# Kernel tuning notes

Measured on AMD Instinct MI355X. Metric: run time of the kernel, lower is better.

The kernel has to match this reference:

```python
import jax, jax.numpy as jnp
import numpy as np

EMBED_DIM = 768
NUM_HEADS = 12
HEAD_DIM = EMBED_DIM // NUM_HEADS
MAX_WAVELENGTH = 10000.0
ROPE_PERCENT = 0.5


def p_rope(x, positions):
    """Partial RoPE (Gemma-style half-split layout) on x: [BH, S, D]."""
    rope_angles = int(ROPE_PERCENT * HEAD_DIM) // 2
    nope_angles = HEAD_DIM // 2 - rope_angles
    fraction = 2.0 * jnp.arange(rope_angles, dtype=x.dtype) / HEAD_DIM
    timescale = MAX_WAVELENGTH ** fraction
    # infinite timescale => angle 0 => identity rotation for the non-roped dims
    timescale = jnp.concatenate([timescale, jnp.full((nope_angles,), jnp.inf, dtype=x.dtype)])
    sinusoid = positions[:, None] / timescale[None, :]  # [S, D/2]
    sin, cos = jnp.sin(sinusoid), jnp.cos(sinusoid)
    x1, x2 = jnp.split(x, 2, axis=-1)  # each [BH, S, D/2]
    return jnp.concatenate([x1 * cos - x2 * sin, x2 * cos + x1 * sin], axis=-1)


def setup_inputs() -> dict:
    key = jax.random.key(0)
    ks = jax.random.split(key, 9)
    B, T, E = 16, 1024, EMBED_DIM
    s = 0.02
    return {
        "hidden_states": jax.random.normal(ks[0], (B, T, E), jnp.float32),
        "wq": jax.random.normal(ks[1], (E, E), jnp.float32) * s,
        "bq": jax.random.normal(ks[2], (E,), jnp.float32) * s,
        "wk": jax.random.normal(ks[3], (E, E), jnp.float32) * s,
        "bk": jax.random.normal(ks[4], (E,), jnp.float32) * s,
        "wv": jax.random.normal(ks[5], (E, E), jnp.float32) * s,
        "bv": jax.random.normal(ks[6], (E,), jnp.float32) * s,
        "wo": jax.random.normal(ks[7], (E, E), jnp.float32) * s,
        "bo": jax.random.normal(ks[8], (E,), jnp.float32) * s,
    }


def _shape(x, B, S):
    # [B, S, E] -> [B*H, S, head_dim]
    return x.reshape(B, S, NUM_HEADS, HEAD_DIM).transpose(0, 2, 1, 3).reshape(B * NUM_HEADS, S, HEAD_DIM)


def reference(hidden_states, wq, bq, wk, bk, wv, bv, wo, bo):
    B, T, E = hidden_states.shape
    scaling = HEAD_DIM ** -0.5
    # torch nn.Linear: y = x @ W.T + b
    q = (hidden_states @ wq.T + bq) * scaling
    k = hidden_states @ wk.T + bk
    v = hidden_states @ wv.T + bv
    q = _shape(q, B, T)  # [BH, T, D]
    k = _shape(k, B, T)
    v = _shape(v, B, T)
    positions = jnp.arange(T, dtype=hidden_states.dtype)
    k = p_rope(k, positions)
    q = p_rope(q, positions)
    attn = jnp.einsum('bqd,bkd->bqk', q, k)  # [BH, T, T]
    attn = jax.nn.softmax(attn, axis=-1)
    out = jnp.einsum('bqk,bkd->bqd', attn, v)  # [BH, T, D]
    out = out.reshape(B, NUM_HEADS, T, HEAD_DIM).transpose(0, 2, 1, 3).reshape(B, T, E)
    return out @ wo.T + bo
```

## Files before the change

kernel.cpp:

```cpp
#include <hip/hip_runtime.h>
#include <hip/hip_bf16.h>
#include <math.h>

typedef __hip_bfloat16 bf16;
typedef __attribute__((ext_vector_type(8))) __bf16 bf16x8;
typedef __attribute__((ext_vector_type(8))) unsigned short u16x8;
typedef __attribute__((ext_vector_type(4))) float f32x4;
typedef __attribute__((ext_vector_type(16))) float f32x16;
typedef unsigned int u32;
typedef __attribute__((ext_vector_type(4))) unsigned int u32x4;

#define DEVI static __device__ __forceinline__

#define BATCH 16
#define SEQ 1024
#define EMB 768
#define NHEAD 12
#define HDIM 64
#define BHEADS (BATCH * NHEAD)
#define MROWS (BATCH * SEQ)

DEVI f32x4 mfma16x16(bf16x8 a, bf16x8 b, f32x4 c) {
  return __builtin_amdgcn_mfma_f32_16x16x32_bf16(a, b, c, 0, 0, 0);
}
DEVI f32x16 mfma32x32(bf16x8 a, bf16x8 b, f32x16 c) {
  return __builtin_amdgcn_mfma_f32_32x32x16_bf16(a, b, c, 0, 0, 0);
}

DEVI void gload_lds16(const bf16* g, void* lds) {
  __builtin_amdgcn_global_load_lds(
      (const __attribute__((address_space(1))) void*)g,
      (__attribute__((address_space(3))) void*)lds, 16, 0, 0);
}

#if __has_builtin(__builtin_amdgcn_exp2f)
DEVI float fexp2(float x) { return __builtin_amdgcn_exp2f(x); }
#else
DEVI float fexp2(float x) { return exp2f(x); }
#endif

DEVI unsigned short f2bf_bits(float f) {
  bf16 h = __float2bfloat16(f);
  return *reinterpret_cast<unsigned short*>(&h);
}
DEVI u32 pack2(float lo, float hi) {
  return (u32)f2bf_bits(lo) | ((u32)f2bf_bits(hi) << 16);
}

__global__ __launch_bounds__(256) void convert_bf16_kernel(
    const float* __restrict__ src, bf16* __restrict__ dst, int n8) {
  int i = blockIdx.x * 256 + threadIdx.x;
  if (i >= n8) return;
  const float4* s = (const float4*)src + (long)i * 2;
  float4 a = s[0], b = s[1];
  u16x8 r;
  r[0] = f2bf_bits(a.x); r[1] = f2bf_bits(a.y);
  r[2] = f2bf_bits(a.z); r[3] = f2bf_bits(a.w);
  r[4] = f2bf_bits(b.x); r[5] = f2bf_bits(b.y);
  r[6] = f2bf_bits(b.z); r[7] = f2bf_bits(b.w);
  *(u16x8*)(dst + (long)i * 8) = r;
}

__global__ __launch_bounds__(256) void convert_w4_kernel(
    const float* __restrict__ s0, const float* __restrict__ s1,
    const float* __restrict__ s2, const float* __restrict__ s3,
    bf16* __restrict__ d0, bf16* __restrict__ d1,
    bf16* __restrict__ d2, bf16* __restrict__ d3, int n8) {
  int i = blockIdx.x * 256 + threadIdx.x;
  if (i >= n8) return;
  const int which = blockIdx.y;
  const float* src = (which == 0) ? s0 : (which == 1) ? s1 : (which == 2) ? s2 : s3;
  bf16* dst = (which == 0) ? d0 : (which == 1) ? d1 : (which == 2) ? d2 : d3;
  const float4* s = (const float4*)src + (long)i * 2;
  float4 a = s[0], b = s[1];
  u16x8 r;
  r[0] = f2bf_bits(a.x); r[1] = f2bf_bits(a.y);
  r[2] = f2bf_bits(a.z); r[3] = f2bf_bits(a.w);
  r[4] = f2bf_bits(b.x); r[5] = f2bf_bits(b.y);
  r[6] = f2bf_bits(b.z); r[7] = f2bf_bits(b.w);
  *(u16x8*)(dst + (long)i * 8) = r;
}

__global__ void rope_table_kernel(float2* __restrict__ tbl) {
  int i = blockIdx.x * 256 + threadIdx.x;
  if (i >= SEQ * 16) return;
  int t = i >> 4;
  int d = i & 15;
  double inv_ts = pow(10000.0, -(double)d / 32.0);
  double ang = (double)t * inv_ts;
  tbl[i] = make_float2((float)cos(ang), (float)sin(ang));
}

DEVI void gemm_core_768(const bf16* __restrict__ A, const bf16* __restrict__ Bt,
                        int rowBase, int colBase, bf16* Asm, bf16* Bsm,
                        f32x4 (&acc)[4][4]) {
  const int K = 768;
  const int NT = 24;
  const int tid = threadIdx.x;
  const int wave = tid >> 6;
  const int lane = tid & 63;
  const int c0 = lane & 15;
  const int khi = lane >> 4;
  const int wm = wave >> 1, wn = wave & 1;
  const int srow = tid >> 2;
  const int scol = ((tid & 3) ^ ((tid >> 3) & 3)) * 8;
  const int sl = (khi ^ ((c0 >> 1) & 3)) * 8;
  const bf16* aG = A + (long)(rowBase + srow) * K + scol;
  const bf16* bG = Bt + (long)(colBase + srow) * K + scol;
  char* aL0 = (char*)Asm + wave * 1024;
  char* aL1 = (char*)Asm + 4096 + wave * 1024;
  char* bL0 = (char*)Bsm + wave * 1024;
  char* bL1 = (char*)Bsm + 4096 + wave * 1024;
  const int stride64 = 64 * K;

#define G_STAGE(boff, kk)                                                    \
  gload_lds16(aG + (kk), aL0 + (boff));                                      \
  gload_lds16(aG + stride64 + (kk), aL1 + (boff));                           \
  gload_lds16(bG + (kk), bL0 + (boff));                                      \
  gload_lds16(bG + stride64 + (kk), bL1 + (boff));

#define G_COMPUTE(be)                                                        \
  {                                                                          \
    bf16x8 af[4], bfr[4];                                                    \
    _Pragma("unroll") for (int m = 0; m < 4; ++m) af[m] =                    \
        *(const bf16x8*)(Asm + (be) + (wm * 64 + m * 16 + c0) * 32 + sl);    \
    _Pragma("unroll") for (int n = 0; n < 4; ++n) bfr[n] =                   \
        *(const bf16x8*)(Bsm + (be) + (wn * 64 + n * 16 + c0) * 32 + sl);    \
    _Pragma("unroll") for (int m = 0; m < 4; ++m)                            \
      _Pragma("unroll") for (int n = 0; n < 4; ++n)                          \
        acc[m][n] = mfma16x16(af[m], bfr[n], acc[m][n]);                     \
  }

#define G_PHASE(beElem, sByte, tc)                                           \
  {                                                                          \
    if ((tc) + 1 < NT) {                                                     \
      asm volatile("s_waitcnt vmcnt(4)" ::: "memory");                       \
    } else {                                                                 \
      asm volatile("s_waitcnt vmcnt(0)" ::: "memory");                       \
    }                                                                        \
    __builtin_amdgcn_s_barrier();                                            \
    __builtin_amdgcn_sched_barrier(0);                                       \
    if ((tc) + 2 < NT) { G_STAGE(sByte, ((tc) + 2) * 32); }                  \
    G_COMPUTE(beElem);                                                       \
  }

  G_STAGE(0, 0);
  G_STAGE(8192, 32);

  for (int tt = 0; tt < NT; tt += 3) {
    G_PHASE(0, 16384, tt);
    G_PHASE(4096, 0, tt + 1);
    G_PHASE(8192, 8192, tt + 2);
  }
#undef G_PHASE
#undef G_STAGE
#undef G_COMPUTE
}

__global__ __launch_bounds__(256, 3) void qkv_kernel(
    const bf16* __restrict__ hs,
    const bf16* __restrict__ wq, const float* __restrict__ bq,
    const bf16* __restrict__ wk, const float* __restrict__ bk,
    const bf16* __restrict__ wv, const float* __restrict__ bv,
    const float2* __restrict__ tbl,
    bf16* __restrict__ Qb, bf16* __restrict__ Kb, bf16* __restrict__ Vtb) {
  __shared__ __align__(16) bf16 Asm[3 * 128 * 32];
  __shared__ __align__(16) bf16 Bsm[3 * 128 * 32];
  const int type = blockIdx.z;
  const bf16* W = (type == 0) ? wq : (type == 1) ? wk : wv;
  const float* bias = (type == 0) ? bq : (type == 1) ? bk : bv;
  const int rowBase = blockIdx.x * 128;
  const int colBase = blockIdx.y * 128;
  f32x4 acc[4][4] = {};
  gemm_core_768(hs, W, rowBase, colBase, Asm, Bsm, acc);

  const int tid = threadIdx.x;
  const int wave = tid >> 6, lane = tid & 63;
  const int c0 = lane & 15, khi = lane >> 4;
  const int wm = wave >> 1, wn = wave & 1;
  const int colW = colBase + wn * 64;
  const int head = colW >> 6;
  float bb[4];
#pragma unroll
  for (int n = 0; n < 4; ++n) bb[n] = bias[colW + n * 16 + c0];

  const int rW = rowBase + wm * 64;
  const int bIdx = rW >> 10;
  const int bh = bIdx * NHEAD + head;

  if (type == 2) {
#pragma unroll
    for (int m = 0; m < 4; ++m) {
      const int t0 = (rW & 1023) + m * 16 + khi * 4;
#pragma unroll
      for (int n = 0; n < 4; ++n) {
        const int d = n * 16 + c0;
        bf16* vp = Vtb + ((long)bh * HDIM + d) * SEQ + t0;
        ushort4 pk;
        pk.x = f2bf_bits(acc[m][n][0] + bb[n]);
        pk.y = f2bf_bits(acc[m][n][1] + bb[n]);
        pk.z = f2bf_bits(acc[m][n][2] + bb[n]);
        pk.w = f2bf_bits(acc[m][n][3] + bb[n]);
        *(ushort4*)vp = pk;
      }
    }
  } else {
    const float scl = (type == 0) ? 0.125f * 1.44269504f : 1.0f;
    bf16* base = ((type == 0) ? Qb : Kb) + (long)bh * SEQ * HDIM;
#pragma unroll
    for (int m = 0; m < 4; ++m) {
#pragma unroll
      for (int ri = 0; ri < 4; ++ri) {
        const int t = (rW & 1023) + m * 16 + khi * 4 + ri;
        float v0 = (acc[m][0][ri] + bb[0]) * scl;
        float v1 = (acc[m][1][ri] + bb[1]) * scl;
        float v2 = (acc[m][2][ri] + bb[2]) * scl;
        float v3 = (acc[m][3][ri] + bb[3]) * scl;
        const float2 cs = tbl[t * 16 + c0];
        const float r0 = v0 * cs.x - v2 * cs.y;
        const float r2 = v2 * cs.x + v0 * cs.y;
        bf16* qp = base + (long)t * HDIM;
        qp[c0] = __float2bfloat16(r0);
        qp[16 + c0] = __float2bfloat16(v1);
        qp[32 + c0] = __float2bfloat16(r2);
        qp[48 + c0] = __float2bfloat16(v3);
      }
    }
  }
}


DEVI int swoff(int row, int s) {
  return row * 128 + (((s ^ (row & 7)) & 7) << 4);
}

__global__ __launch_bounds__(256, 2) void attn_kernel(
    const bf16* __restrict__ Q, const bf16* __restrict__ K,
    const bf16* __restrict__ Vt, bf16* __restrict__ Ao) {
  __shared__ __align__(16) char smem[4 * 8192];
  const int bid = blockIdx.x;
  const int xcd = bid & 7, idx = bid >> 3;
  const int bh = xcd + ((idx >> 2) << 3);
  const int qt = idx & 3;

  const int tid = threadIdx.x;
  const int lane = tid & 63;
  const int w = tid >> 6;
  const int l31 = lane & 31;
  const int hi = lane >> 5;

  const bf16* Qh = Q + (long)bh * SEQ * HDIM;
  const bf16* Kh = K + (long)bh * SEQ * HDIM;
  const bf16* Vh = Vt + (long)bh * HDIM * SEQ;

  const int qbase = qt * 256 + w * 64;
  bf16x8 qf[2][4];
#pragma unroll
  for (int qn = 0; qn < 2; ++qn)
#pragma unroll
    for (int ks = 0; ks < 4; ++ks)
      qf[qn][ks] = *(const bf16x8*)(Qh + (qbase + qn * 32 + l31) * HDIM +
                                    ks * 16 + hi * 8);

  f32x16 o[2][2] = {};
  float lacc[2] = {0.f, 0.f};

  const int sr = tid >> 3;
  const int sc = tid & 7;

  bf16x8 kr0 = *(const bf16x8*)(Kh + sr * HDIM + sc * 8);
  bf16x8 kr1 = *(const bf16x8*)(Kh + (sr + 32) * HDIM + sc * 8);
  bf16x8 vr0 = *(const bf16x8*)(Vh + sr * SEQ + sc * 8);
  bf16x8 vr1 = *(const bf16x8*)(Vh + (sr + 32) * SEQ + sc * 8);
  *(bf16x8*)(smem + swoff(sr, sc)) = kr0;
  *(bf16x8*)(smem + swoff(sr + 32, sc)) = kr1;
  *(bf16x8*)(smem + 16384 + swoff(sr, sc)) = vr0;
  *(bf16x8*)(smem + 16384 + swoff(sr + 32, sc)) = vr1;
  __syncthreads();

  for (int ct = 0; ct < SEQ / 64; ++ct) {
    const int co = (ct & 1) * 8192;
    const char* Kc = smem + co;
    const char* Vc = smem + 16384 + co;

    if (ct != 15) {
      const int nt = (ct + 1) * 64;
      kr0 = *(const bf16x8*)(Kh + (nt + sr) * HDIM + sc * 8);
      kr1 = *(const bf16x8*)(Kh + (nt + sr + 32) * HDIM + sc * 8);
      vr0 = *(const bf16x8*)(Vh + sr * SEQ + nt + sc * 8);
      vr1 = *(const bf16x8*)(Vh + (sr + 32) * SEQ + nt + sc * 8);
    }

    f32x16 s[2][2] = {};
#pragma unroll
    for (int m = 0; m < 2; ++m)
#pragma unroll
      for (int ks = 0; ks < 4; ++ks) {
        bf16x8 ka = *(const bf16x8*)(Kc + swoff(m * 32 + l31, ks * 2 + hi));
        s[m][0] = mfma32x32(ka, qf[0][ks], s[m][0]);
        s[m][1] = mfma32x32(ka, qf[1][ks], s[m][1]);
      }

    bf16x8 pf[2][4];
#pragma unroll
    for (int qn = 0; qn < 2; ++qn) {
      u32 wds[2][4][2];
#pragma unroll
      for (int m = 0; m < 2; ++m)
#pragma unroll
        for (int b = 0; b < 4; ++b)
#pragma unroll
          for (int pp = 0; pp < 2; ++pp) {
            const float p0 = fexp2(s[m][qn][4 * b + 2 * pp]);
            const float p1 = fexp2(s[m][qn][4 * b + 2 * pp + 1]);
            lacc[qn] += p0 + p1;
            wds[m][b][pp] = pack2(p0, p1);
          }
#pragma unroll
      for (int m = 0; m < 2; ++m)
#pragma unroll
        for (int ts = 0; ts < 2; ++ts) {
          u32 x0 = wds[m][2 * ts][0], y0 = wds[m][2 * ts + 1][0];
          u32 x1 = wds[m][2 * ts][1], y1 = wds[m][2 * ts + 1][1];
          asm("v_permlane32_swap_b32 %0, %1" : "+v"(x0), "+v"(y0));
          asm("v_permlane32_swap_b32 %0, %1" : "+v"(x1), "+v"(y1));
          u32x4 t = {x0, x1, y0, y1};
          pf[qn][2 * m + ts] = *(bf16x8*)&t;
        }
    }

#pragma unroll
    for (int dm = 0; dm < 2; ++dm)
#pragma unroll
      for (int tk = 0; tk < 4; ++tk) {
        bf16x8 va = *(const bf16x8*)(Vc + swoff(dm * 32 + l31, tk * 2 + hi));
        o[dm][0] = mfma32x32(va, pf[0][tk], o[dm][0]);
        o[dm][1] = mfma32x32(va, pf[1][tk], o[dm][1]);
      }

    if (ct != 15) {
      const int no = 8192 - co;
      *(bf16x8*)(smem + no + swoff(sr, sc)) = kr0;
      *(bf16x8*)(smem + no + swoff(sr + 32, sc)) = kr1;
      *(bf16x8*)(smem + 16384 + no + swoff(sr, sc)) = vr0;
      *(bf16x8*)(smem + 16384 + no + swoff(sr + 32, sc)) = vr1;
      __syncthreads();
    }
  }

#pragma unroll
  for (int qn = 0; qn < 2; ++qn) lacc[qn] += __shfl_xor(lacc[qn], 32);
  const float inv0 = 1.0f / lacc[0];
  const float inv1 = 1.0f / lacc[1];

  const int bb = bh / NHEAD;
  const int hh = bh % NHEAD;
#pragma unroll
  for (int qn = 0; qn < 2; ++qn) {
    const float inv = qn ? inv1 : inv0;
    const int t = qbase + qn * 32 + l31;
    bf16* orow = Ao + (long)(bb * SEQ + t) * EMB + hh * HDIM;
#pragma unroll
    for (int dm = 0; dm < 2; ++dm)
#pragma unroll
      for (int b = 0; b < 4; ++b)
#pragma unroll
        for (int pp = 0; pp < 2; ++pp) {
          const int r = 4 * b + 2 * pp;
          const int d = dm * 32 + 2 * pp + 8 * b + 4 * hi;
          *(u32*)(orow + d) = pack2(o[dm][qn][r] * inv, o[dm][qn][r + 1] * inv);
        }
  }
}

__global__ __launch_bounds__(256, 3) void oproj_kernel(
    const bf16* __restrict__ X, const bf16* __restrict__ wo,
    const float* __restrict__ bo, float* __restrict__ out) {
  __shared__ __align__(16) bf16 Asm[3 * 128 * 32];
  __shared__ __align__(16) bf16 Bsm[3 * 128 * 32];
  const int rowBase = blockIdx.x * 128;
  const int colBase = blockIdx.y * 128;
  f32x4 acc[4][4] = {};
  gemm_core_768(X, wo, rowBase, colBase, Asm, Bsm, acc);
  const int tid = threadIdx.x;
  const int wave = tid >> 6, lane = tid & 63;
  const int c0 = lane & 15, khi = lane >> 4;
  const int wm = wave >> 1, wn = wave & 1;
  const int colW = colBase + wn * 64;
  float bb[4];
#pragma unroll
  for (int n = 0; n < 4; ++n) bb[n] = bo[colW + n * 16 + c0];
#pragma unroll
  for (int m = 0; m < 4; ++m)
#pragma unroll
    for (int ri = 0; ri < 4; ++ri) {
      const int row = rowBase + wm * 64 + m * 16 + khi * 4 + ri;
      float* op = out + (long)row * EMB + colW;
#pragma unroll
      for (int n = 0; n < 4; ++n)
        op[n * 16 + c0] = acc[m][n][ri] + bb[n];
    }
}

extern "C" void kernel_launch(void* const* d_in, const int* in_sizes, int n_in,
                              void* d_out, int out_size, void* d_ws, size_t ws_size,
                              hipStream_t stream) {
  const float* hs_f = (const float*)d_in[0];
  const float* wq_f = (const float*)d_in[1];
  const float* bq = (const float*)d_in[2];
  const float* wk_f = (const float*)d_in[3];
  const float* bk = (const float*)d_in[4];
  const float* wv_f = (const float*)d_in[5];
  const float* bv = (const float*)d_in[6];
  const float* wo_f = (const float*)d_in[7];
  const float* bo = (const float*)d_in[8];
  float* out = (float*)d_out;

  char* ws = (char*)d_ws;
  size_t off = 0;
  float2* tbl = (float2*)ws; off += 131072;
  const size_t hsBytes = (size_t)MROWS * EMB * 2;
  const size_t wBytes = (size_t)EMB * EMB * 2;
  const size_t bufBytes = (size_t)BHEADS * SEQ * HDIM * 2;
  bf16* hsb = (bf16*)(ws + off); off += hsBytes;
  bf16* wqb = (bf16*)(ws + off); off += wBytes;
  bf16* wkb = (bf16*)(ws + off); off += wBytes;
  bf16* wvb = (bf16*)(ws + off); off += wBytes;
  bf16* wob = (bf16*)(ws + off); off += wBytes;
  bf16* Qb = (bf16*)(ws + off); off += bufBytes;
  bf16* Kb = (bf16*)(ws + off); off += bufBytes;
  bf16* Vtb = (bf16*)(ws + off); off += bufBytes;
  bf16* Ao = (bf16*)(ws + off);

  const int nHs8 = MROWS * EMB / 8;
  const int nW8 = EMB * EMB / 8;
  convert_bf16_kernel<<<dim3(nHs8 / 256), dim3(256), 0, stream>>>(hs_f, hsb, nHs8);
  convert_w4_kernel<<<dim3(nW8 / 256, 4), dim3(256), 0, stream>>>(
      wq_f, wk_f, wv_f, wo_f, wqb, wkb, wvb, wob, nW8);
  rope_table_kernel<<<dim3(64), dim3(256), 0, stream>>>(tbl);
  qkv_kernel<<<dim3(MROWS / 128, EMB / 128, 3), dim3(256), 0, stream>>>(
      hsb, wqb, bq, wkb, bk, wvb, bv, tbl, Qb, Kb, Vtb);
  attn_kernel<<<dim3(768), dim3(256), 0, stream>>>(Qb, Kb, Vtb, Ao);
  oproj_kernel<<<dim3(MROWS / 128, EMB / 128), dim3(256), 0, stream>>>(Ao, wob, bo, out);
}
```

Measured before the change: 186.0 us.

## Widen GEMM tiles to 128x256 with per-wave 128x64 and prioritize attention MFMAs

```diff
diff --git a/kernel.cpp b/kernel.cpp
--- a/kernel.cpp
+++ b/kernel.cpp
@@ -93,7 +93,7 @@
 
 DEVI void gemm_core_768(const bf16* __restrict__ A, const bf16* __restrict__ Bt,
                         int rowBase, int colBase, bf16* Asm, bf16* Bsm,
-                        f32x4 (&acc)[4][4]) {
+                        f32x4 (&acc)[8][4]) {
   const int K = 768;
   const int NT = 24;
   const int tid = threadIdx.x;
@@ -101,63 +101,67 @@
   const int lane = tid & 63;
   const int c0 = lane & 15;
   const int khi = lane >> 4;
-  const int wm = wave >> 1, wn = wave & 1;
   const int srow = tid >> 2;
   const int scol = ((tid & 3) ^ ((tid >> 3) & 3)) * 8;
   const int sl = (khi ^ ((c0 >> 1) & 3)) * 8;
   const bf16* aG = A + (long)(rowBase + srow) * K + scol;
   const bf16* bG = Bt + (long)(colBase + srow) * K + scol;
   char* aL0 = (char*)Asm + wave * 1024;
-  char* aL1 = (char*)Asm + 4096 + wave * 1024;
+  char* aL1 = aL0 + 4096;
   char* bL0 = (char*)Bsm + wave * 1024;
-  char* bL1 = (char*)Bsm + 4096 + wave * 1024;
-  const int stride64 = 64 * K;
-
-#define G_STAGE(boff, kk)                                                    \
-  gload_lds16(aG + (kk), aL0 + (boff));                                      \
-  gload_lds16(aG + stride64 + (kk), aL1 + (boff));                           \
-  gload_lds16(bG + (kk), bL0 + (boff));                                      \
-  gload_lds16(bG + stride64 + (kk), bL1 + (boff));
-
-#define G_COMPUTE(be)                                                        \
+  char* bL1 = bL0 + 4096;
+  char* bL2 = bL0 + 8192;
+  char* bL3 = bL0 + 12288;
+  const int s64 = 64 * K, s128 = 128 * K, s192 = 192 * K;
+
+#define G_STAGE(aB, bB, kk)                                                  \
+  gload_lds16(aG + (kk), aL0 + (aB));                                        \
+  gload_lds16(aG + s64 + (kk), aL1 + (aB));                                  \
+  gload_lds16(bG + (kk), bL0 + (bB));                                        \
+  gload_lds16(bG + s64 + (kk), bL1 + (bB));                                  \
+  gload_lds16(bG + s128 + (kk), bL2 + (bB));                                 \
+  gload_lds16(bG + s192 + (kk), bL3 + (bB));
+
+#define G_COMPUTE(aE, bE)                                                    \
   {                                                                          \
-    bf16x8 af[4], bfr[4];                                                    \
-    _Pragma("unroll") for (int m = 0; m < 4; ++m) af[m] =                    \
-        *(const bf16x8*)(Asm + (be) + (wm * 64 + m * 16 + c0) * 32 + sl);    \
+    bf16x8 bfr[4];                                                           \
     _Pragma("unroll") for (int n = 0; n < 4; ++n) bfr[n] =                   \
-        *(const bf16x8*)(Bsm + (be) + (wn * 64 + n * 16 + c0) * 32 + sl);    \
-    _Pragma("unroll") for (int m = 0; m < 4; ++m)                            \
+        *(const bf16x8*)(Bsm + (bE) + (wave * 64 + n * 16 + c0) * 32 + sl);  \
+    _Pragma("unroll") for (int m = 0; m < 8; ++m) {                          \
+      bf16x8 af =                                                            \
+          *(const bf16x8*)(Asm + (aE) + (m * 16 + c0) * 32 + sl);            \
       _Pragma("unroll") for (int n = 0; n < 4; ++n)                          \
-        acc[m][n] = mfma16x16(af[m], bfr[n], acc[m][n]);                     \
-  }
-
-#define G_PHASE(beElem, sByte, tc)                                           \
+          acc[m][n] = mfma16x16(af, bfr[n], acc[m][n]);                      \
+    }                                                                        \
+  }
+
+#define G_PHASE(aE, bE, aS, bS, tc)                                          \
   {                                                                          \
     if ((tc) + 1 < NT) {                                                     \
-      asm volatile("s_waitcnt vmcnt(4)" ::: "memory");                       \
+      asm volatile("s_waitcnt vmcnt(6)" ::: "memory");                       \
     } else {                                                                 \
       asm volatile("s_waitcnt vmcnt(0)" ::: "memory");                       \
     }                                                                        \
     __builtin_amdgcn_s_barrier();                                            \
     __builtin_amdgcn_sched_barrier(0);                                       \
-    if ((tc) + 2 < NT) { G_STAGE(sByte, ((tc) + 2) * 32); }                  \
-    G_COMPUTE(beElem);                                                       \
-  }
-
-  G_STAGE(0, 0);
-  G_STAGE(8192, 32);
+    if ((tc) + 2 < NT) { G_STAGE(aS, bS, ((tc) + 2) * 32); }                 \
+    G_COMPUTE(aE, bE);                                                       \
+  }
+
+  G_STAGE(0, 0, 0);
+  G_STAGE(8192, 16384, 32);
 
   for (int tt = 0; tt < NT; tt += 3) {
-    G_PHASE(0, 16384, tt);
-    G_PHASE(4096, 0, tt + 1);
-    G_PHASE(8192, 8192, tt + 2);
+    G_PHASE(0, 0, 16384, 32768, tt);
+    G_PHASE(4096, 8192, 0, 0, tt + 1);
+    G_PHASE(8192, 16384, 8192, 16384, tt + 2);
   }
 #undef G_PHASE
 #undef G_STAGE
 #undef G_COMPUTE
 }
 
-__global__ __launch_bounds__(256, 3) void qkv_kernel(
+__global__ __launch_bounds__(256, 2) void qkv_kernel(
     const bf16* __restrict__ hs,
     const bf16* __restrict__ wq, const float* __restrict__ bq,
     const bf16* __restrict__ wk, const float* __restrict__ bk,
@@ -165,33 +169,32 @@
     const float2* __restrict__ tbl,
     bf16* __restrict__ Qb, bf16* __restrict__ Kb, bf16* __restrict__ Vtb) {
   __shared__ __align__(16) bf16 Asm[3 * 128 * 32];
-  __shared__ __align__(16) bf16 Bsm[3 * 128 * 32];
+  __shared__ __align__(16) bf16 Bsm[3 * 256 * 32];
   const int type = blockIdx.z;
   const bf16* W = (type == 0) ? wq : (type == 1) ? wk : wv;
   const float* bias = (type == 0) ? bq : (type == 1) ? bk : bv;
   const int rowBase = blockIdx.x * 128;
-  const int colBase = blockIdx.y * 128;
-  f32x4 acc[4][4] = {};
+  const int colBase = blockIdx.y * 256;
+  f32x4 acc[8][4] = {};
   gemm_core_768(hs, W, rowBase, colBase, Asm, Bsm, acc);
 
   const int tid = threadIdx.x;
   const int wave = tid >> 6, lane = tid & 63;
   const int c0 = lane & 15, khi = lane >> 4;
-  const int wm = wave >> 1, wn = wave & 1;
-  const int colW = colBase + wn * 64;
+  const int colW = colBase + wave * 64;
   const int head = colW >> 6;
   float bb[4];
 #pragma unroll
   for (int n = 0; n < 4; ++n) bb[n] = bias[colW + n * 16 + c0];
 
-  const int rW = rowBase + wm * 64;
-  const int bIdx = rW >> 10;
+  const int bIdx = rowBase >> 10;
   const int bh = bIdx * NHEAD + head;
+  const int rT = rowBase & 1023;
 
   if (type == 2) {
 #pragma unroll
-    for (int m = 0; m < 4; ++m) {
-      const int t0 = (rW & 1023) + m * 16 + khi * 4;
+    for (int m = 0; m < 8; ++m) {
+      const int t0 = rT + m * 16 + khi * 4;
 #pragma unroll
       for (int n = 0; n < 4; ++n) {
         const int d = n * 16 + c0;
@@ -208,10 +211,10 @@
     const float scl = (type == 0) ? 0.125f * 1.44269504f : 1.0f;
     bf16* base = ((type == 0) ? Qb : Kb) + (long)bh * SEQ * HDIM;
 #pragma unroll
-    for (int m = 0; m < 4; ++m) {
+    for (int m = 0; m < 8; ++m) {
 #pragma unroll
       for (int ri = 0; ri < 4; ++ri) {
-        const int t = (rW & 1023) + m * 16 + khi * 4 + ri;
+        const int t = rT + m * 16 + khi * 4 + ri;
         float v0 = (acc[m][0][ri] + bb[0]) * scl;
         float v1 = (acc[m][1][ri] + bb[1]) * scl;
         float v2 = (acc[m][2][ri] + bb[2]) * scl;
@@ -292,6 +295,7 @@
     }
 
     f32x16 s[2][2] = {};
+    __builtin_amdgcn_s_setprio(1);
 #pragma unroll
     for (int m = 0; m < 2; ++m)
 #pragma unroll
@@ -300,6 +304,7 @@
         s[m][0] = mfma32x32(ka, qf[0][ks], s[m][0]);
         s[m][1] = mfma32x32(ka, qf[1][ks], s[m][1]);
       }
+    __builtin_amdgcn_s_setprio(0);
 
     bf16x8 pf[2][4];
 #pragma unroll
@@ -329,6 +334,7 @@
         }
     }
 
+    __builtin_amdgcn_s_setprio(1);
 #pragma unroll
     for (int dm = 0; dm < 2; ++dm)
 #pragma unroll
@@ -337,6 +343,7 @@
         o[dm][0] = mfma32x32(va, pf[0][tk], o[dm][0]);
         o[dm][1] = mfma32x32(va, pf[1][tk], o[dm][1]);
       }
+    __builtin_amdgcn_s_setprio(0);
 
     if (ct != 15) {
       const int no = 8192 - co;
@@ -373,28 +380,27 @@
   }
 }
 
-__global__ __launch_bounds__(256, 3) void oproj_kernel(
+__global__ __launch_bounds__(256, 2) void oproj_kernel(
     const bf16* __restrict__ X, const bf16* __restrict__ wo,
     const float* __restrict__ bo, float* __restrict__ out) {
   __shared__ __align__(16) bf16 Asm[3 * 128 * 32];
-  __shared__ __align__(16) bf16 Bsm[3 * 128 * 32];
+  __shared__ __align__(16) bf16 Bsm[3 * 256 * 32];
   const int rowBase = blockIdx.x * 128;
-  const int colBase = blockIdx.y * 128;
-  f32x4 acc[4][4] = {};
+  const int colBase = blockIdx.y * 256;
+  f32x4 acc[8][4] = {};
   gemm_core_768(X, wo, rowBase, colBase, Asm, Bsm, acc);
   const int tid = threadIdx.x;
   const int wave = tid >> 6, lane = tid & 63;
   const int c0 = lane & 15, khi = lane >> 4;
-  const int wm = wave >> 1, wn = wave & 1;
-  const int colW = colBase + wn * 64;
+  const int colW = colBase + wave * 64;
   float bb[4];
 #pragma unroll
   for (int n = 0; n < 4; ++n) bb[n] = bo[colW + n * 16 + c0];
 #pragma unroll
-  for (int m = 0; m < 4; ++m)
+  for (int m = 0; m < 8; ++m)
 #pragma unroll
     for (int ri = 0; ri < 4; ++ri) {
-      const int row = rowBase + wm * 64 + m * 16 + khi * 4 + ri;
+      const int row = rowBase + m * 16 + khi * 4 + ri;
       float* op = out + (long)row * EMB + colW;
 #pragma unroll
       for (int n = 0; n < 4; ++n)
@@ -438,8 +444,8 @@
   convert_w4_kernel<<<dim3(nW8 / 256, 4), dim3(256), 0, stream>>>(
       wq_f, wk_f, wv_f, wo_f, wqb, wkb, wvb, wob, nW8);
   rope_table_kernel<<<dim3(64), dim3(256), 0, stream>>>(tbl);
-  qkv_kernel<<<dim3(MROWS / 128, EMB / 128, 3), dim3(256), 0, stream>>>(
+  qkv_kernel<<<dim3(MROWS / 128, EMB / 256, 3), dim3(256), 0, stream>>>(
       hsb, wqb, bq, wkb, bk, wvb, bv, tbl, Qb, Kb, Vtb);
   attn_kernel<<<dim3(768), dim3(256), 0, stream>>>(Qb, Kb, Vtb, Ao);
-  oproj_kernel<<<dim3(MROWS / 128, EMB / 128), dim3(256), 0, stream>>>(Ao, wob, bo, out);
-}
+  oproj_kernel<<<dim3(MROWS / 128, EMB / 256), dim3(256), 0, stream>>>(Ao, wob, bo, out);
+}
```

New measurement: 203.9 us. +9.6%, slower.
